# Kernel optimization log

Measured on AMD Instinct MI355X. Metric: run time of the kernel, lower is better.

The kernel has to match this reference:

```python
import jax, jax.numpy as jnp
import numpy as np

B, T, L, H, W = 8, 30000, 6, 128, 128
D_IN, C_DIM, HID, Z_DIM = 3, 32, 256, 128
MAX_DIM = 0.55


def setup_inputs() -> dict:
    key = jax.random.key(0)
    ks = jax.random.split(key, 12)
    p = jax.random.uniform(ks[0], (B, T, D_IN), dtype=jnp.float32)
    z = jax.random.normal(ks[1], (B, Z_DIM), dtype=jnp.float32)
    c = jax.random.normal(ks[2], (B, L, H, W, C_DIM), dtype=jnp.float32)
    # camera-like matrices: small rotation rows so projected coords stay in [-1, 1]
    C_mat = (jax.random.uniform(ks[3], (B, L, 4, 3), dtype=jnp.float32) - 0.5) * 0.3
    C_mat = C_mat.at[:, :, 3, :].set(1.0)  # row used as projection denominator
    fc_p_w = jax.random.normal(ks[4], (HID, D_IN), dtype=jnp.float32) * 0.1
    fc_p_b = jnp.zeros((HID,), jnp.float32)
    blk0_w0 = jax.random.normal(ks[5], (C_DIM, HID), dtype=jnp.float32) * 0.05
    blk0_b0 = jnp.zeros((C_DIM,), jnp.float32)
    blk0_w1 = jax.random.normal(ks[6], (C_DIM, C_DIM), dtype=jnp.float32) * 0.1
    blk0_b1 = jnp.zeros((C_DIM,), jnp.float32)
    blk0_ws = jax.random.normal(ks[7], (C_DIM, HID), dtype=jnp.float32) * 0.05
    blk_w0 = jax.random.normal(ks[8], (4, C_DIM, C_DIM), dtype=jnp.float32) * 0.1
    blk_b0 = jnp.zeros((4, C_DIM), jnp.float32)
    blk_w1 = jax.random.normal(ks[9], (4, C_DIM, C_DIM), dtype=jnp.float32) * 0.1
    blk_b1 = jnp.zeros((4, C_DIM), jnp.float32)
    fc_out_w = jax.random.normal(ks[10], (1, C_DIM), dtype=jnp.float32) * 0.1
    fc_out_b = jnp.zeros((1,), jnp.float32)
    return dict(p=p, z=z, c=c, C_mat=C_mat, fc_p_w=fc_p_w, fc_p_b=fc_p_b,
                blk0_w0=blk0_w0, blk0_b0=blk0_b0, blk0_w1=blk0_w1, blk0_b1=blk0_b1,
                blk0_ws=blk0_ws, blk_w0=blk_w0, blk_b0=blk_b0, blk_w1=blk_w1,
                blk_b1=blk_b1, fc_out_w=fc_out_w, fc_out_b=fc_out_b)


def _bilinear(p, c, C_mat):
    # p: [B,T,3], c: [B,L,H,W,D], C_mat: [B,L,4,3]
    Bb, Ll, Hh, Ww, Dd = c.shape
    interval = 2.0 / (Hh - 1)
    pp = p / MAX_DIM
    # proj[b,l,t,i] = sum_j C_mat[b,l,i,j] * pp[b,t,j]
    proj = jnp.einsum('blij,btj->blti', C_mat[:, :, :3, :], pp)
    denom = C_mat[:, :, 3, 0] + 0.05                      # [B,L]
    proj = proj / denom[:, :, None, None]
    xy = (proj[..., :2] + 1.0) / interval                 # [B,L,T,2]
    x, y = xy[..., 0], xy[..., 1]
    x0f, x1f = jnp.floor(x), jnp.ceil(x)
    y0f, y1f = jnp.floor(y), jnp.ceil(y)
    dx = (x1f - x)[..., None]                             # [B,L,T,1]
    dy = (y1f - y)[..., None]
    x0 = jnp.clip(x0f.astype(jnp.int32), 0, Hh - 1)
    x1 = jnp.clip(x1f.astype(jnp.int32), 0, Hh - 1)
    y0 = jnp.clip(y0f.astype(jnp.int32), 0, Ww - 1)
    y1 = jnp.clip(y1f.astype(jnp.int32), 0, Ww - 1)
    bi = jnp.arange(Bb)[:, None, None]
    li = jnp.arange(Ll)[None, :, None]
    f11 = c[bi, li, x0, y0]                               # [B,L,T,D]
    f12 = c[bi, li, x1, y0]
    f21 = c[bi, li, x0, y1]
    f22 = c[bi, li, x1, y1]
    interp = (f11 * dx * dy + f12 * (1 - dx) * dy
              + f21 * dx * (1 - dy) + f22 * (1 - dx) * (1 - dy))
    return interp.sum(axis=1)                             # sum over views -> [B,T,D]


def reference(p, z, c, C_mat, fc_p_w, fc_p_b, blk0_w0, blk0_b0, blk0_w1, blk0_b1,
              blk0_ws, blk_w0, blk_b0, blk_w1, blk_b1, fc_out_w, fc_out_b):
    feat = _bilinear(p, c, C_mat)                         # [B,T,32]
    net = p @ fc_p_w.T + fc_p_b                           # 1x1 conv == linear, [B,T,256]
    # block0 (256 -> 32, with linear shortcut)
    h = jax.nn.relu(net) @ blk0_w0.T + blk0_b0
    dx_ = jax.nn.relu(h) @ blk0_w1.T + blk0_b1
    net = net @ blk0_ws.T + dx_
    net = net + feat
    # blocks 1..4 (32 -> 32, identity shortcut)
    for i in range(4):
        h = jax.nn.relu(net) @ blk_w0[i].T + blk_b0[i]
        net = net + (jax.nn.relu(h) @ blk_w1[i].T + blk_b1[i])
        net = net + feat
    out = jax.nn.relu(net) @ fc_out_w.T + fc_out_b        # [B,T,1]
    return out[..., 0]                                    # [B,T]
```

## Files before the change

### kernel.cpp

```cpp
#include <hip/hip_runtime.h>

#define NB 8
#define NT 30000
#define NL 6
#define NC 32
#define NHID 256

typedef _Float16 f16;
typedef f16 half8 __attribute__((ext_vector_type(8)));
typedef f16 half4v __attribute__((ext_vector_type(4)));
typedef f16 half2v __attribute__((ext_vector_type(2)));
typedef float floatx4 __attribute__((ext_vector_type(4)));

#define C_ELEMS (25165824ull)
#define NCONV   12288
#define FEAT_ELEMS (7680000ull)

#define OFF_W0A  0
#define OFF_WA   8192
#define OFF_HB   17408
#define OFF_FOLD 18432
#define OFF_F32  18560
#define IMG_F16  19456

__device__ __align__(16) f16 g_chalf[C_ELEMS];
__device__ __align__(16) f16 g_feat[FEAT_ELEMS];
__device__ __align__(16) f16 g_img[IMG_F16];

__device__ __forceinline__ int permrow(int m) {
    return 8 * ((m & 15) >> 2) + 4 * (m >> 4) + (m & 3);
}

__device__ __forceinline__ half2v cvt2(float a, float b) {
    return __builtin_bit_cast(half2v, __builtin_amdgcn_cvt_pkrtz(a, b));
}

__device__ __forceinline__ half8 pack8(floatx4 f0, floatx4 f1) {
    half2v h0 = cvt2(f0[0], f0[1]), h1 = cvt2(f0[2], f0[3]);
    half2v h2 = cvt2(f1[0], f1[1]), h3 = cvt2(f1[2], f1[3]);
    half4v q0 = __builtin_shufflevector(h0, h1, 0, 1, 2, 3);
    half4v q1 = __builtin_shufflevector(h2, h3, 0, 1, 2, 3);
    return __builtin_shufflevector(q0, q1, 0, 1, 2, 3, 4, 5, 6, 7);
}

__device__ __forceinline__ half8 relupack2(floatx4 a, floatx4 b) {
    half2v p0 = cvt2(fmaxf(a[0], 0.f), fmaxf(a[1], 0.f));
    half2v p1 = cvt2(fmaxf(a[2], 0.f), fmaxf(a[3], 0.f));
    half2v p2 = cvt2(fmaxf(b[0], 0.f), fmaxf(b[1], 0.f));
    half2v p3 = cvt2(fmaxf(b[2], 0.f), fmaxf(b[3], 0.f));
    half4v q0 = __builtin_shufflevector(p0, p1, 0, 1, 2, 3);
    half4v q1 = __builtin_shufflevector(p2, p3, 0, 1, 2, 3);
    return __builtin_shufflevector(q0, q1, 0, 1, 2, 3, 4, 5, 6, 7);
}

__device__ __forceinline__ half8 zext4(half4v lo) {
    const half4v zh = {};
    return __builtin_shufflevector(lo, zh, 0, 1, 2, 3, 4, 5, 6, 7);
}

__device__ __forceinline__ half8 splat8(float w) {
    f16 h = (f16)w;
    half8 v = {h, h, h, h, h, h, h, h};
    return v;
}

__global__ __launch_bounds__(256) void convert_prep(
    const float* __restrict__ c,
    const float* __restrict__ fpw, const float* __restrict__ fpb,
    const float* __restrict__ b0w0, const float* __restrict__ b0b0,
    const float* __restrict__ b0w1, const float* __restrict__ b0b1,
    const float* __restrict__ b0ws, const float* __restrict__ bw0,
    const float* __restrict__ bb0, const float* __restrict__ bw1,
    const float* __restrict__ bb1, const float* __restrict__ fow,
    const float* __restrict__ fob)
{
    __shared__ floatx4 sp[8][32];
    const int tid = threadIdx.x;
    if (blockIdx.x < NCONV) {
        size_t i = ((size_t)blockIdx.x * 256 + tid) * 8;
        floatx4 f0 = *(const floatx4*)(c + i);
        floatx4 f1 = *(const floatx4*)(c + i + 4);
        *(half8*)(g_chalf + i) = pack8(f0, f1);
        return;
    }
    {
        int i = tid & 31, kc = tid >> 5;
        const float* wrow = b0ws + i * 256 + kc * 32;
        const float* pw = fpw + kc * 96;
        const float* pb = fpb + kc * 32;
        floatx4 acc = {};
        #pragma unroll 8
        for (int k = 0; k < 32; k++) {
            float w = wrow[k];
            acc[0] = fmaf(w, pw[k * 3 + 0], acc[0]);
            acc[1] = fmaf(w, pw[k * 3 + 1], acc[1]);
            acc[2] = fmaf(w, pw[k * 3 + 2], acc[2]);
            acc[3] = fmaf(w, pb[k], acc[3]);
        }
        sp[kc][i] = acc;
    }
    __syncthreads();
    {
        int m = tid >> 3, seg = tid & 7;
        const float* src = b0w0 + permrow(m) * 256 + seg * 32;
        f16* dst = g_img + OFF_W0A + m * 256;
        int sw = m & 7;
        #pragma unroll
        for (int ci = 0; ci < 4; ci++) {
            int cidx = seg * 4 + ci;
            floatx4 f0 = *(const floatx4*)(src + ci * 8);
            floatx4 f1 = *(const floatx4*)(src + ci * 8 + 4);
            *(half8*)(dst + ((cidx ^ sw) << 3)) = pack8(f0, f1);
        }
    }
    for (int r = tid; r < 288; r += 256) {
        int mi = r >> 5, m = r & 31;
        int pm = permrow(m);
        const float* src;
        if (mi == 0) src = b0w1 + pm * 32;
        else {
            int mat = mi - 1, bi = mat >> 1;
            src = ((mat & 1) ? bw1 : bw0) + (bi * 32 + pm) * 32;
        }
        f16* dst = g_img + OFF_WA + mi * 1024 + m * 32;
        int sw = (m >> 1) & 3;
        #pragma unroll
        for (int ci = 0; ci < 4; ci++) {
            floatx4 f0 = *(const floatx4*)(src + ci * 8);
            floatx4 f1 = *(const floatx4*)(src + ci * 8 + 4);
            *(half8*)(dst + ((ci ^ sw) << 3)) = pack8(f0, f1);
        }
    }
    {
        int cch = tid >> 5, m = tid & 31;
        int h = cch * 32 + permrow(m);
        half2v a = cvt2(fpw[h * 3 + 0], fpw[h * 3 + 1]);
        half2v bq = cvt2(fpw[h * 3 + 2], fpb[h]);
        *(half4v*)(g_img + OFF_HB + tid * 4) = __builtin_shufflevector(a, bq, 0, 1, 2, 3);
    }
    float* fimg = (float*)(g_img + OFF_F32);
    if (tid < 32) {
        int pm = permrow(tid);
        floatx4 s = sp[0][pm];
        #pragma unroll
        for (int j = 1; j < 8; j++) s += sp[j][pm];
        half2v a = cvt2(s[0], s[1]);
        half2v bq = cvt2(s[2], s[3] + b0b1[pm]);
        *(half4v*)(g_img + OFF_FOLD + tid * 4) = __builtin_shufflevector(a, bq, 0, 1, 2, 3);
        fimg[tid] = b0b0[tid];
        fimg[32 + tid] = fow[tid];
    }
    if (tid >= 64 && tid < 192) {
        fimg[tid] = bb0[tid - 64];
        fimg[tid + 128] = bb1[tid - 64];
    }
    if (tid == 0) fimg[320] = fob[0];
}

__global__ __launch_bounds__(256, 4) void gather_kernel(
    const float* __restrict__ p, const float* __restrict__ Cm)
{
    __shared__ float s_cam[NL][8];
    const int tid = threadIdx.x;
    const int b = blockIdx.x & 7;
    const int tile = blockIdx.x >> 3;

    if (tid < NL) {
        const float* cm = Cm + ((size_t)b * NL + tid) * 12;
        float denom = cm[9] + 0.05f;
        float s = 63.5f / (0.55f * denom);
        s_cam[tid][0] = cm[0] * s; s_cam[tid][1] = cm[1] * s; s_cam[tid][2] = cm[2] * s;
        s_cam[tid][3] = cm[3] * s; s_cam[tid][4] = cm[4] * s; s_cam[tid][5] = cm[5] * s;
    }
    __syncthreads();

    const int lane = tid & 63;
    const int wv = tid >> 6;
    const int q = lane >> 4;
    const int i16 = lane & 15;
    const f16* cqh = g_chalf + (((size_t)b * NL) << 19) + q * 8;

    #pragma unroll 1
    for (int g = 0; g < 2; g++) {
        const int t = tile * 128 + (g * 4 + wv) * 16 + i16;
        const int tc = min(t, NT - 1);
        const float* pp = p + ((size_t)b * NT + tc) * 3;
        float px = pp[0], py = pp[1], pz = pp[2];

        half8 feh = {};
        #pragma unroll
        for (int l = 0; l < NL; l++) {
            float x = s_cam[l][0] * px + s_cam[l][1] * py + s_cam[l][2] * pz + 63.5f;
            float y = s_cam[l][3] * px + s_cam[l][4] * py + s_cam[l][5] * pz + 63.5f;
            float x0f = floorf(x), x1f = ceilf(x);
            float y0f = floorf(y), y1f = ceilf(y);
            float dxw = x1f - x, dyw = y1f - y;
            int x0 = min(max((int)x0f, 0), 127);
            int x1 = min(max((int)x1f, 0), 127);
            int y0 = min(max((int)y0f, 0), 127);
            int y1 = min(max((int)y1f, 0), 127);
            const f16* base = cqh + ((size_t)l << 19);
            half8 t11 = *(const half8*)(base + (size_t)((x0 << 7) + y0) * 32);
            half8 t12 = *(const half8*)(base + (size_t)((x1 << 7) + y0) * 32);
            half8 t21 = *(const half8*)(base + (size_t)((x0 << 7) + y1) * 32);
            half8 t22 = *(const half8*)(base + (size_t)((x1 << 7) + y1) * 32);
            float w11 = dxw * dyw;
            float w12 = (1.f - dxw) * dyw;
            float w21 = dxw * (1.f - dyw);
            float w22 = (1.f - dxw) * (1.f - dyw);
            feh += t11 * splat8(w11) + t12 * splat8(w12)
                 + t21 * splat8(w21) + t22 * splat8(w22);
        }
        if (t < NT)
            *(half8*)(g_feat + ((size_t)b * NT + t) * 32 + q * 8) = feh;
    }
}

__global__ __launch_bounds__(256, 2) void mlp_kernel(
    const float* __restrict__ p, float* __restrict__ out)
{
    __shared__ __align__(16) f16 s_img[IMG_F16];
    const int tid = threadIdx.x;
    const int b = blockIdx.x & 7;
    const int tile = blockIdx.x >> 3;

    {
        const uint4* gsrc = (const uint4*)g_img;
        uint4* ldst = (uint4*)s_img;
        for (int i = tid; i < IMG_F16 / 8; i += 256) ldst[i] = gsrc[i];
    }
    __syncthreads();

    const int lane = tid & 63;
    const int wv = tid >> 6;
    const int q = lane >> 4;
    const int i16 = lane & 15;
    const int sw0 = i16 & 7;

    const f16* s_w0A = s_img + OFF_W0A;
    const f16* s_wA  = s_img + OFF_WA;
    const f16* s_hB  = s_img + OFF_HB;
    const float* sf  = (const float*)(s_img + OFF_F32);

    const f16* w0r0 = s_w0A + i16 * 256;
    const f16* w0r1 = s_w0A + (16 + i16) * 256;
    const int qsw = (q ^ ((i16 >> 1) & 3)) << 3;
    const int soff0 = i16 * 32 + qsw;
    const int soff1 = (16 + i16) * 32 + qsw;
    const f16* hB0 = s_hB + i16 * 4;
    const f16* hB1 = s_hB + (16 + i16) * 4;

    const half8 fA0 = zext4(*(const half4v*)(s_img + OFF_FOLD + i16 * 4));
    const half8 fA1 = zext4(*(const half4v*)(s_img + OFF_FOLD + (16 + i16) * 4));
    const floatx4 fw0 = *(const floatx4*)&sf[32 + q * 8];
    const floatx4 fw1 = *(const floatx4*)&sf[32 + q * 8 + 4];
    const floatx4 b00a = *(const floatx4*)&sf[q * 8];
    const floatx4 b00b = *(const floatx4*)&sf[q * 8 + 4];
    const float fobv = sf[320];

    #pragma unroll 1
    for (int g = 0; g < 2; g++) {
        const int t = tile * 128 + (g * 4 + wv) * 16 + i16;
        const int tc = min(t, NT - 1);
        const float* pp = p + ((size_t)b * NT + tc) * 3;
        float px = pp[0], py = pp[1], pz = pp[2];

        half8 feh = *(const half8*)(g_feat + ((size_t)b * NT + tc) * 32 + q * 8);
        floatx4 fe0 = floatx4{(float)feh[0], (float)feh[1], (float)feh[2], (float)feh[3]};
        floatx4 fe1 = floatx4{(float)feh[4], (float)feh[5], (float)feh[6], (float)feh[7]};

        half8 bp;
        {
            half2v xy = cvt2(px, py), z1 = cvt2(pz, 1.0f);
            half4v lo = __builtin_shufflevector(xy, z1, 0, 1, 2, 3);
            half8 full = zext4(lo);
            const half8 zh8 = {};
            bp = (q == 0) ? full : zh8;
        }

        floatx4 acc0 = b00a, acc1 = b00b;
        #pragma unroll 2
        for (int cch = 0; cch < 8; cch++) {
            half8 ha = zext4(*(const half4v*)(hB0 + cch * 128));
            half8 hb = zext4(*(const half4v*)(hB1 + cch * 128));
            floatx4 hz = {};
            floatx4 h0 = __builtin_amdgcn_mfma_f32_16x16x32_f16(ha, bp, hz, 0, 0, 0);
            floatx4 h1 = __builtin_amdgcn_mfma_f32_16x16x32_f16(hb, bp, hz, 0, 0, 0);
            half8 bf = relupack2(h0, h1);
            half8 a0 = *(const half8*)(w0r0 + ((((cch << 2) | q) ^ sw0) << 3));
            half8 a1 = *(const half8*)(w0r1 + ((((cch << 2) | q) ^ sw0) << 3));
            acc0 = __builtin_amdgcn_mfma_f32_16x16x32_f16(a0, bf, acc0, 0, 0, 0);
            acc1 = __builtin_amdgcn_mfma_f32_16x16x32_f16(a1, bf, acc1, 0, 0, 0);
        }

        floatx4 st0 = __builtin_amdgcn_mfma_f32_16x16x32_f16(fA0, bp, fe0, 0, 0, 0);
        floatx4 st1 = __builtin_amdgcn_mfma_f32_16x16x32_f16(fA1, bp, fe1, 0, 0, 0);
        {
            half8 bf = relupack2(acc0, acc1);
            half8 a0 = *(const half8*)(s_wA + soff0);
            half8 a1 = *(const half8*)(s_wA + soff1);
            st0 = __builtin_amdgcn_mfma_f32_16x16x32_f16(a0, bf, st0, 0, 0, 0);
            st1 = __builtin_amdgcn_mfma_f32_16x16x32_f16(a1, bf, st1, 0, 0, 0);
        }

        #pragma unroll
        for (int bk = 0; bk < 4; bk++) {
            const f16* w_a = s_wA + (1 + 2 * bk) * 1024;
            const f16* w_b = s_wA + (2 + 2 * bk) * 1024;
            floatx4 h0 = *(const floatx4*)&sf[64 + bk * 32 + q * 8];
            floatx4 h1 = *(const floatx4*)&sf[64 + bk * 32 + q * 8 + 4];
            {
                half8 bf = relupack2(st0, st1);
                half8 a0 = *(const half8*)(w_a + soff0);
                half8 a1 = *(const half8*)(w_a + soff1);
                h0 = __builtin_amdgcn_mfma_f32_16x16x32_f16(a0, bf, h0, 0, 0, 0);
                h1 = __builtin_amdgcn_mfma_f32_16x16x32_f16(a1, bf, h1, 0, 0, 0);
            }
            floatx4 d0 = *(const floatx4*)&sf[192 + bk * 32 + q * 8];
            floatx4 d1 = *(const floatx4*)&sf[192 + bk * 32 + q * 8 + 4];
            {
                half8 bf = relupack2(h0, h1);
                half8 a0 = *(const half8*)(w_b + soff0);
                half8 a1 = *(const half8*)(w_b + soff1);
                d0 = __builtin_amdgcn_mfma_f32_16x16x32_f16(a0, bf, d0, 0, 0, 0);
                d1 = __builtin_amdgcn_mfma_f32_16x16x32_f16(a1, bf, d1, 0, 0, 0);
            }
            st0 += d0 + fe0;
            st1 += d1 + fe1;
        }

        float o = 0.f;
        #pragma unroll
        for (int r = 0; r < 4; r++)
            o += fmaxf(st0[r], 0.f) * fw0[r] + fmaxf(st1[r], 0.f) * fw1[r];
        o += __shfl_xor(o, 16);
        o += __shfl_xor(o, 32);
        if (q == 0 && t < NT) out[(size_t)b * NT + t] = o + fobv;
    }
}

extern "C" void kernel_launch(void* const* d_in, const int* in_sizes, int n_in,
                              void* d_out, int out_size, void* d_ws, size_t ws_size,
                              hipStream_t stream) {
    const float* p    = (const float*)d_in[0];
    const float* c    = (const float*)d_in[2];
    const float* Cm   = (const float*)d_in[3];
    const float* fpw  = (const float*)d_in[4];
    const float* fpb  = (const float*)d_in[5];
    const float* b0w0 = (const float*)d_in[6];
    const float* b0b0 = (const float*)d_in[7];
    const float* b0w1 = (const float*)d_in[8];
    const float* b0b1 = (const float*)d_in[9];
    const float* b0ws = (const float*)d_in[10];
    const float* bw0  = (const float*)d_in[11];
    const float* bb0  = (const float*)d_in[12];
    const float* bw1  = (const float*)d_in[13];
    const float* bb1  = (const float*)d_in[14];
    const float* fow  = (const float*)d_in[15];
    const float* fob  = (const float*)d_in[16];

    convert_prep<<<NCONV + 1, 256, 0, stream>>>(c, fpw, fpb, b0w0, b0b0, b0w1, b0b1,
                                                b0ws, bw0, bb0, bw1, bb1, fow, fob);

    dim3 grid(((NT + 127) / 128) * NB);
    gather_kernel<<<grid, 256, 0, stream>>>(p, Cm);
    mlp_kernel<<<grid, 256, 0, stream>>>(p, (float*)d_out);
}
```

Measured before the change: 254.9 us.

## Split gather across view halves and smaller tiles for more parallelism

The gather kernel now splits the six camera views into two halves, each handled by separate blocks over 64-point tiles, and writes two partial feature buffers. The MLP kernel loads both partial buffers and sums them. The goal is more blocks in flight and higher occupancy (launch bounds raised to 6) to hide the latency of the random bilinear gathers. The cost is twice the feature write/read traffic, recomputing the point loads per half, and an extra fp16 add that adds rounding.

```diff
diff --git a/kernel.cpp b/kernel.cpp
--- a/kernel.cpp
+++ b/kernel.cpp
@@ -14,7 +14,9 @@
 
 #define C_ELEMS (25165824ull)
 #define NCONV   12288
-#define FEAT_ELEMS (7680000ull)
+#define FEAT_HALF (7680000ull)
+#define GTILES  469
+#define GHALF   (GTILES * 8)
 
 #define OFF_W0A  0
 #define OFF_WA   8192
@@ -24,7 +26,7 @@
 #define IMG_F16  19456
 
 __device__ __align__(16) f16 g_chalf[C_ELEMS];
-__device__ __align__(16) f16 g_feat[FEAT_ELEMS];
+__device__ __align__(16) f16 g_feat[2 * FEAT_HALF];
 __device__ __align__(16) f16 g_img[IMG_F16];
 
 __device__ __forceinline__ int permrow(int m) {
@@ -157,16 +159,18 @@
     if (tid == 0) fimg[320] = fob[0];
 }
 
-__global__ __launch_bounds__(256, 4) void gather_kernel(
+__global__ __launch_bounds__(256, 6) void gather_kernel(
     const float* __restrict__ p, const float* __restrict__ Cm)
 {
-    __shared__ float s_cam[NL][8];
+    __shared__ float s_cam[3][8];
     const int tid = threadIdx.x;
-    const int b = blockIdx.x & 7;
-    const int tile = blockIdx.x >> 3;
-
-    if (tid < NL) {
-        const float* cm = Cm + ((size_t)b * NL + tid) * 12;
+    const int half = blockIdx.x / GHALF;
+    const int rem = blockIdx.x - half * GHALF;
+    const int tile = rem >> 3;
+    const int b = rem & 7;
+
+    if (tid < 3) {
+        const float* cm = Cm + ((size_t)b * NL + half * 3 + tid) * 12;
         float denom = cm[9] + 0.05f;
         float s = 63.5f / (0.55f * denom);
         s_cam[tid][0] = cm[0] * s; s_cam[tid][1] = cm[1] * s; s_cam[tid][2] = cm[2] * s;
@@ -178,42 +182,39 @@
     const int wv = tid >> 6;
     const int q = lane >> 4;
     const int i16 = lane & 15;
-    const f16* cqh = g_chalf + (((size_t)b * NL) << 19) + q * 8;
-
-    #pragma unroll 1
-    for (int g = 0; g < 2; g++) {
-        const int t = tile * 128 + (g * 4 + wv) * 16 + i16;
-        const int tc = min(t, NT - 1);
-        const float* pp = p + ((size_t)b * NT + tc) * 3;
-        float px = pp[0], py = pp[1], pz = pp[2];
-
-        half8 feh = {};
-        #pragma unroll
-        for (int l = 0; l < NL; l++) {
-            float x = s_cam[l][0] * px + s_cam[l][1] * py + s_cam[l][2] * pz + 63.5f;
-            float y = s_cam[l][3] * px + s_cam[l][4] * py + s_cam[l][5] * pz + 63.5f;
-            float x0f = floorf(x), x1f = ceilf(x);
-            float y0f = floorf(y), y1f = ceilf(y);
-            float dxw = x1f - x, dyw = y1f - y;
-            int x0 = min(max((int)x0f, 0), 127);
-            int x1 = min(max((int)x1f, 0), 127);
-            int y0 = min(max((int)y0f, 0), 127);
-            int y1 = min(max((int)y1f, 0), 127);
-            const f16* base = cqh + ((size_t)l << 19);
-            half8 t11 = *(const half8*)(base + (size_t)((x0 << 7) + y0) * 32);
-            half8 t12 = *(const half8*)(base + (size_t)((x1 << 7) + y0) * 32);
-            half8 t21 = *(const half8*)(base + (size_t)((x0 << 7) + y1) * 32);
-            half8 t22 = *(const half8*)(base + (size_t)((x1 << 7) + y1) * 32);
-            float w11 = dxw * dyw;
-            float w12 = (1.f - dxw) * dyw;
-            float w21 = dxw * (1.f - dyw);
-            float w22 = (1.f - dxw) * (1.f - dyw);
-            feh += t11 * splat8(w11) + t12 * splat8(w12)
-                 + t21 * splat8(w21) + t22 * splat8(w22);
-        }
-        if (t < NT)
-            *(half8*)(g_feat + ((size_t)b * NT + t) * 32 + q * 8) = feh;
-    }
+    const f16* cqh = g_chalf + ((((size_t)b * NL + half * 3)) << 19) + q * 8;
+
+    const int t = tile * 64 + wv * 16 + i16;
+    const int tc = min(t, NT - 1);
+    const float* pp = p + ((size_t)b * NT + tc) * 3;
+    float px = pp[0], py = pp[1], pz = pp[2];
+
+    half8 feh = {};
+    #pragma unroll
+    for (int l = 0; l < 3; l++) {
+        float x = s_cam[l][0] * px + s_cam[l][1] * py + s_cam[l][2] * pz + 63.5f;
+        float y = s_cam[l][3] * px + s_cam[l][4] * py + s_cam[l][5] * pz + 63.5f;
+        float x0f = floorf(x), x1f = ceilf(x);
+        float y0f = floorf(y), y1f = ceilf(y);
+        float dxw = x1f - x, dyw = y1f - y;
+        int x0 = min(max((int)x0f, 0), 127);
+        int x1 = min(max((int)x1f, 0), 127);
+        int y0 = min(max((int)y0f, 0), 127);
+        int y1 = min(max((int)y1f, 0), 127);
+        const f16* base = cqh + ((size_t)l << 19);
+        half8 t11 = *(const half8*)(base + (size_t)((x0 << 7) + y0) * 32);
+        half8 t12 = *(const half8*)(base + (size_t)((x1 << 7) + y0) * 32);
+        half8 t21 = *(const half8*)(base + (size_t)((x0 << 7) + y1) * 32);
+        half8 t22 = *(const half8*)(base + (size_t)((x1 << 7) + y1) * 32);
+        float w11 = dxw * dyw;
+        float w12 = (1.f - dxw) * dyw;
+        float w21 = dxw * (1.f - dyw);
+        float w22 = (1.f - dxw) * (1.f - dyw);
+        feh += t11 * splat8(w11) + t12 * splat8(w12)
+             + t21 * splat8(w21) + t22 * splat8(w22);
+    }
+    if (t < NT)
+        *(half8*)(g_feat + half * FEAT_HALF + ((size_t)b * NT + t) * 32 + q * 8) = feh;
 }
 
 __global__ __launch_bounds__(256, 2) void mlp_kernel(
@@ -265,7 +266,10 @@
         const float* pp = p + ((size_t)b * NT + tc) * 3;
         float px = pp[0], py = pp[1], pz = pp[2];
 
-        half8 feh = *(const half8*)(g_feat + ((size_t)b * NT + tc) * 32 + q * 8);
+        const f16* fbase = g_feat + ((size_t)b * NT + tc) * 32 + q * 8;
+        half8 fh0 = *(const half8*)(fbase);
+        half8 fh1 = *(const half8*)(fbase + FEAT_HALF);
+        half8 feh = fh0 + fh1;
         floatx4 fe0 = floatx4{(float)feh[0], (float)feh[1], (float)feh[2], (float)feh[3]};
         floatx4 fe1 = floatx4{(float)feh[4], (float)feh[5], (float)feh[6], (float)feh[7]};
 
@@ -362,7 +366,8 @@
     convert_prep<<<NCONV + 1, 256, 0, stream>>>(c, fpw, fpb, b0w0, b0b0, b0w1, b0b1,
                                                 b0ws, bw0, bb0, bw1, bb1, fow, fob);
 
+    gather_kernel<<<2 * GHALF, 256, 0, stream>>>(p, Cm);
+
     dim3 grid(((NT + 127) / 128) * NB);
-    gather_kernel<<<grid, 256, 0, stream>>>(p, Cm);
     mlp_kernel<<<grid, 256, 0, stream>>>(p, (float*)d_out);
 }
```

Result: no change. 252.4 us (-1.0%).
